# Kernel optimization log

Hardware: AMD Instinct MI355X
Metric: run time of the kernel (lower is better)

## Reference

```python
import jax, jax.numpy as jnp
import numpy as np

N = 100000      # nodes
E = 1600000     # edges (avg degree 16)
D_IN, D_H, D_Z = 128, 64, 32
BN_EPS = 1e-5


def setup_inputs() -> dict:
    key = jax.random.key(0)
    ks = jax.random.split(key, 16)
    lin = lambda k, i, o: jax.random.normal(k, (i, o), jnp.float32) / np.sqrt(i).astype(np.float32)
    return {
        "x": jax.random.normal(ks[0], (N, D_IN), jnp.float32),
        "edge_index": jax.random.randint(ks[1], (2, E), 0, N),
        "edge_attr": jax.random.uniform(ks[2], (E,), jnp.float32),
        "W_in": lin(ks[3], D_IN, D_H), "b_in": jnp.zeros((D_H,), jnp.float32),
        "W1": lin(ks[4], D_H, D_H),   "b1": jnp.zeros((D_H,), jnp.float32),
        "W2": lin(ks[5], D_H, D_H),   "b2": jnp.zeros((D_H,), jnp.float32),
        "Wmu": lin(ks[6], D_H, D_Z),  "bmu": jnp.zeros((D_Z,), jnp.float32),
        "Wlv": lin(ks[7], D_H, D_Z),  "blv": jnp.zeros((D_Z,), jnp.float32),
        "g1": jnp.ones((D_H,), jnp.float32), "be1": jnp.zeros((D_H,), jnp.float32),
        "g2": jnp.ones((D_H,), jnp.float32), "be2": jnp.zeros((D_H,), jnp.float32),
    }


def gcn_conv(h, W, b, src, dst, ew):
    # standard GCNConv: linear transform, then sym-normalized weighted aggregation
    # with self-loops of weight 1.
    h = h @ W + b                                   # [N, F_out]
    deg = jax.ops.segment_sum(ew, dst, num_segments=N) + 1.0   # self-loop -> deg >= 1
    dinv = jax.lax.rsqrt(deg)                       # [N]
    coef = dinv[src] * dinv[dst] * ew               # [E]
    agg = jax.ops.segment_sum(h[src] * coef[:, None], dst, num_segments=N)
    return agg + h * (dinv * dinv)[:, None]         # add self-loop contribution


def batch_norm(h, g, b):
    m = h.mean(axis=0)
    v = h.var(axis=0)
    return g * (h - m) * jax.lax.rsqrt(v + BN_EPS) + b


def reference(x, edge_index, edge_attr, W_in, b_in, W1, b1, W2, b2,
              Wmu, bmu, Wlv, blv, g1, be1, g2, be2):
    src, dst = edge_index[0], edge_index[1]
    h = x @ W_in + b_in
    h = gcn_conv(h, W1, b1, src, dst, edge_attr)
    h = jax.nn.relu(batch_norm(h, g1, be1))         # dropout = identity (eval)
    h = gcn_conv(h, W2, b2, src, dst, edge_attr)
    h = jax.nn.relu(batch_norm(h, g2, be2))
    mu = gcn_conv(h, Wmu, bmu, src, dst, edge_attr)
    logvar = gcn_conv(h, Wlv, blv, src, dst, edge_attr)
    return (mu, logvar)
```

## Files before the change

kernel.cpp:

```cpp
#include <hip/hip_runtime.h>

#define NN 100000
#define NE 1600000

__global__ __launch_bounds__(256) void k_degpack(const int* __restrict__ dst,
    const float* __restrict__ ew, unsigned long long* __restrict__ packed,
    unsigned char* __restrict__ rank) {
  int e = blockIdx.x * 256 + threadIdx.x;
  if (e < NE) {
    int d = dst[e];
    unsigned long long rec = (1ULL << 40) |
        (unsigned long long)__float2uint_rn(ew[e] * 16777216.0f);
    unsigned long long old = atomicAdd(&packed[d], rec);
    rank[e] = (unsigned char)(old >> 40);
  }
}

__global__ __launch_bounds__(256) void k_unpack(const unsigned long long* __restrict__ packed,
    float* __restrict__ dinv, int* __restrict__ cnt) {
  int i = blockIdx.x * 256 + threadIdx.x;
  if (i < NN) {
    unsigned long long v = packed[i];
    cnt[i] = (int)(v >> 40);
    float deg = (float)(v & ((1ULL << 40) - 1)) * (1.0f / 16777216.0f);
    dinv[i] = rsqrtf(deg + 1.0f);
  }
}

__global__ __launch_bounds__(256) void k_scan1(const int* __restrict__ cnt,
    int* __restrict__ indptr, int* __restrict__ bsum) {
  __shared__ int sd[256];
  int t = threadIdx.x, i = blockIdx.x * 256 + t;
  int v = (i < NN) ? cnt[i] : 0;
  sd[t] = v; __syncthreads();
  #pragma unroll
  for (int o = 1; o < 256; o <<= 1) {
    int x = (t >= o) ? sd[t - o] : 0;
    __syncthreads(); sd[t] += x; __syncthreads();
  }
  if (i < NN) indptr[i] = sd[t] - v;
  if (t == 255) bsum[blockIdx.x] = sd[255];
}

__global__ __launch_bounds__(512) void k_scan2(const int* __restrict__ bsum,
    int* __restrict__ boff, int nb) {
  __shared__ int sd[512];
  int t = threadIdx.x;
  int v = (t < nb) ? bsum[t] : 0;
  sd[t] = v; __syncthreads();
  #pragma unroll
  for (int o = 1; o < 512; o <<= 1) {
    int x = (t >= o) ? sd[t - o] : 0;
    __syncthreads(); sd[t] += x; __syncthreads();
  }
  if (t < nb) boff[t] = sd[t] - v;
}

__global__ __launch_bounds__(256) void k_scan3(int* __restrict__ indptr,
    const int* __restrict__ boff) {
  int i = blockIdx.x * 256 + threadIdx.x;
  if (i < NN) {
    indptr[i] = indptr[i] + boff[i >> 8];
  } else if (i == NN) {
    indptr[NN] = NE;
  }
}

__global__ __launch_bounds__(256) void k_fill(const int* __restrict__ src,
    const int* __restrict__ dst, const float* __restrict__ ew,
    const float* __restrict__ dinv, const int* __restrict__ indptr,
    const unsigned char* __restrict__ rank, int2* __restrict__ edges) {
  int e = blockIdx.x * 256 + threadIdx.x;
  if (e < NE) {
    int s = src[e], d = dst[e];
    int p = indptr[d] + (int)rank[e];
    float coef = dinv[s] * dinv[d] * ew[e];
    edges[p] = make_int2(s, __float_as_int(coef));
  }
}

template<int K, int RPT, bool BN>
__global__ __launch_bounds__(256) void k_lin(const float* __restrict__ in,
    const float* __restrict__ W, const float* __restrict__ bias,
    const float* __restrict__ stats, const float* __restrict__ g,
    const float* __restrict__ be, float* __restrict__ out) {
  constexpr int ROWS = 16 * RPT, RS = ROWS + 4;
  __shared__ __align__(16) float Wl[K * 64];
  __shared__ __align__(16) float rlT[K * RS];
  __shared__ __align__(16) float bl[64];
  __shared__ float bnscale[BN ? K : 1], bnshift[BN ? K : 1];
  int t = threadIdx.x;
  int r0 = blockIdx.x * ROWS;
  for (int i = t; i < K * 64; i += 256) Wl[i] = W[i];
  if (t < 64) bl[t] = bias[t];
  if constexpr (BN) {
    if (t < K) {
      const float invn = 1.0f / (float)NN;
      float m = stats[t] * invn;
      float v = stats[64 + t] * invn - m * m;
      float sc = g[t] * rsqrtf(v + 1e-5f);
      bnscale[t] = sc;
      bnshift[t] = be[t] - m * sc;
    }
    __syncthreads();
  }
  for (int i = t; i < ROWS * K; i += 256) {
    int r = i / K, k = i - r * K;
    int row = r0 + r;
    float v = (row < NN) ? in[(size_t)row * K + k] : 0.f;
    if constexpr (BN) {
      v = v * bnscale[k] + bnshift[k];
      v = v > 0.f ? v : 0.f;
    }
    rlT[k * RS + r] = v;
  }
  __syncthreads();
  int tc = t & 15, tr = t >> 4;
  float4 bv = *(const float4*)&bl[tc * 4];
  float acc[RPT][4];
  #pragma unroll
  for (int j = 0; j < RPT; j++) { acc[j][0] = bv.x; acc[j][1] = bv.y; acc[j][2] = bv.z; acc[j][3] = bv.w; }
  for (int k = 0; k < K; k++) {
    float4 wv = *(const float4*)&Wl[k * 64 + tc * 4];
    float rv[RPT];
    if constexpr (RPT == 4) {
      float4 r4 = *(const float4*)&rlT[k * RS + tr * 4];
      rv[0] = r4.x; rv[1] = r4.y; rv[2] = r4.z; rv[3] = r4.w;
    } else {
      float2 r2 = *(const float2*)&rlT[k * RS + tr * 2];
      rv[0] = r2.x; rv[1] = r2.y;
    }
    #pragma unroll
    for (int j = 0; j < RPT; j++) {
      acc[j][0] += rv[j] * wv.x;
      acc[j][1] += rv[j] * wv.y;
      acc[j][2] += rv[j] * wv.z;
      acc[j][3] += rv[j] * wv.w;
    }
  }
  #pragma unroll
  for (int j = 0; j < RPT; j++) {
    int row = r0 + tr * RPT + j;
    if (row < NN) {
      float4 o = make_float4(acc[j][0], acc[j][1], acc[j][2], acc[j][3]);
      *(float4*)&out[(size_t)row * 64 + tc * 4] = o;
    }
  }
}

__global__ __launch_bounds__(256) void k_linz(const float* __restrict__ in,
    const float* __restrict__ Wmu, const float* __restrict__ bmu,
    const float* __restrict__ Wlv, const float* __restrict__ blv,
    const float* __restrict__ stats, const float* __restrict__ g,
    const float* __restrict__ be, float* __restrict__ out) {
  constexpr int K = 64, RPT = 4, ROWS = 64, RS = 68;
  __shared__ __align__(16) float Wl[K * 64];
  __shared__ __align__(16) float rlT[K * RS];
  __shared__ __align__(16) float bl[64];
  __shared__ float bnscale[K], bnshift[K];
  int t = threadIdx.x;
  int r0 = blockIdx.x * ROWS;
  for (int i = t; i < K * 64; i += 256) {
    int k = i >> 6, c = i & 63;
    Wl[i] = (c < 32) ? Wmu[k * 32 + c] : Wlv[k * 32 + c - 32];
  }
  if (t < 64) bl[t] = (t < 32) ? bmu[t] : blv[t - 32];
  if (t < K) {
    const float invn = 1.0f / (float)NN;
    float m = stats[t] * invn;
    float v = stats[64 + t] * invn - m * m;
    float sc = g[t] * rsqrtf(v + 1e-5f);
    bnscale[t] = sc;
    bnshift[t] = be[t] - m * sc;
  }
  __syncthreads();
  for (int i = t; i < ROWS * K; i += 256) {
    int r = i / K, k = i - r * K;
    int row = r0 + r;
    float v = (row < NN) ? in[(size_t)row * K + k] : 0.f;
    v = v * bnscale[k] + bnshift[k];
    rlT[k * RS + r] = v > 0.f ? v : 0.f;
  }
  __syncthreads();
  int tc = t & 15, tr = t >> 4;
  float4 bv = *(const float4*)&bl[tc * 4];
  float acc[RPT][4];
  #pragma unroll
  for (int j = 0; j < RPT; j++) { acc[j][0] = bv.x; acc[j][1] = bv.y; acc[j][2] = bv.z; acc[j][3] = bv.w; }
  for (int k = 0; k < K; k++) {
    float4 wv = *(const float4*)&Wl[k * 64 + tc * 4];
    float4 r4 = *(const float4*)&rlT[k * RS + tr * 4];
    float rv[4] = { r4.x, r4.y, r4.z, r4.w };
    #pragma unroll
    for (int j = 0; j < RPT; j++) {
      acc[j][0] += rv[j] * wv.x;
      acc[j][1] += rv[j] * wv.y;
      acc[j][2] += rv[j] * wv.z;
      acc[j][3] += rv[j] * wv.w;
    }
  }
  #pragma unroll
  for (int j = 0; j < RPT; j++) {
    int row = r0 + tr * RPT + j;
    if (row < NN) {
      float4 o = make_float4(acc[j][0], acc[j][1], acc[j][2], acc[j][3]);
      *(float4*)&out[(size_t)row * 64 + tc * 4] = o;
    }
  }
}

template<bool FINAL>
__global__ __launch_bounds__(256) void k_gather2(const float2* __restrict__ h,
    const float* __restrict__ dinv, const int* __restrict__ indptr,
    const int2* __restrict__ edges, float* __restrict__ out) {
  int wid = (blockIdx.x * 256 + threadIdx.x) >> 6;
  int lane = threadIdx.x & 63;
  int half = lane >> 5, sub = lane & 31;
  int i = wid * 2 + half;
  if (i >= NN) return;
  int e0 = indptr[i], e1 = indptr[i + 1];
  float di = dinv[i];
  float2 hv = h[(size_t)i * 32 + sub];
  float2 acc = make_float2(hv.x * di * di, hv.y * di * di);
  int e = e0;
  for (; e + 8 <= e1; e += 8) {
    int2 r0 = edges[e];
    int2 r1 = edges[e + 1];
    int2 r2 = edges[e + 2];
    int2 r3 = edges[e + 3];
    int2 r4 = edges[e + 4];
    int2 r5 = edges[e + 5];
    int2 r6 = edges[e + 6];
    int2 r7 = edges[e + 7];
    float2 v0 = h[(size_t)r0.x * 32 + sub];
    float2 v1 = h[(size_t)r1.x * 32 + sub];
    float2 v2 = h[(size_t)r2.x * 32 + sub];
    float2 v3 = h[(size_t)r3.x * 32 + sub];
    float2 v4 = h[(size_t)r4.x * 32 + sub];
    float2 v5 = h[(size_t)r5.x * 32 + sub];
    float2 v6 = h[(size_t)r6.x * 32 + sub];
    float2 v7 = h[(size_t)r7.x * 32 + sub];
    float c0 = __int_as_float(r0.y), c1 = __int_as_float(r1.y);
    float c2 = __int_as_float(r2.y), c3 = __int_as_float(r3.y);
    float c4 = __int_as_float(r4.y), c5 = __int_as_float(r5.y);
    float c6 = __int_as_float(r6.y), c7 = __int_as_float(r7.y);
    acc.x += v0.x * c0; acc.y += v0.y * c0;
    acc.x += v1.x * c1; acc.y += v1.y * c1;
    acc.x += v2.x * c2; acc.y += v2.y * c2;
    acc.x += v3.x * c3; acc.y += v3.y * c3;
    acc.x += v4.x * c4; acc.y += v4.y * c4;
    acc.x += v5.x * c5; acc.y += v5.y * c5;
    acc.x += v6.x * c6; acc.y += v6.y * c6;
    acc.x += v7.x * c7; acc.y += v7.y * c7;
  }
  for (; e + 2 <= e1; e += 2) {
    int2 ra = edges[e];
    int2 rb = edges[e + 1];
    float2 va = h[(size_t)ra.x * 32 + sub];
    float2 vb = h[(size_t)rb.x * 32 + sub];
    float ca = __int_as_float(ra.y), cb = __int_as_float(rb.y);
    acc.x += va.x * ca; acc.y += va.y * ca;
    acc.x += vb.x * cb; acc.y += vb.y * cb;
  }
  if (e < e1) {
    int2 r = edges[e];
    float2 v = h[(size_t)r.x * 32 + sub];
    float c = __int_as_float(r.y);
    acc.x += v.x * c; acc.y += v.y * c;
  }
  if (!FINAL) {
    *(float2*)&out[(size_t)i * 64 + sub * 2] = acc;
  } else {
    int c0 = sub * 2;
    if (sub < 16) {
      *(float2*)&out[(size_t)i * 32 + c0] = acc;
    } else {
      *(float2*)&out[(size_t)NN * 32 + (size_t)i * 32 + (c0 - 32)] = acc;
    }
  }
}

__global__ __launch_bounds__(256) void k_bnstats(const float* __restrict__ h,
    float* __restrict__ stats) {
  __shared__ float s1[256], s2[256];
  int t = threadIdx.x, c = t & 63, rg = t >> 6;
  float a1 = 0.f, a2 = 0.f;
  for (int row = blockIdx.x * 4 + rg; row < NN; row += gridDim.x * 4) {
    float v = h[(size_t)row * 64 + c];
    a1 += v; a2 += v * v;
  }
  s1[t] = a1; s2[t] = a2; __syncthreads();
  if (rg == 0) {
    a1 = s1[c] + s1[64 + c] + s1[128 + c] + s1[192 + c];
    a2 = s2[c] + s2[64 + c] + s2[128 + c] + s2[192 + c];
    atomicAdd(&stats[c], a1);
    atomicAdd(&stats[64 + c], a2);
  }
}

extern "C" void kernel_launch(void* const* d_in, const int* in_sizes, int n_in,
                              void* d_out, int out_size, void* d_ws, size_t ws_size,
                              hipStream_t stream) {
  (void)in_sizes; (void)n_in; (void)out_size; (void)ws_size;
  const float* x    = (const float*)d_in[0];
  const int*   ei   = (const int*)d_in[1];
  const float* ew   = (const float*)d_in[2];
  const float* W_in = (const float*)d_in[3];
  const float* b_in = (const float*)d_in[4];
  const float* W1   = (const float*)d_in[5];
  const float* b1   = (const float*)d_in[6];
  const float* W2   = (const float*)d_in[7];
  const float* b2   = (const float*)d_in[8];
  const float* Wmu  = (const float*)d_in[9];
  const float* bmu  = (const float*)d_in[10];
  const float* Wlv  = (const float*)d_in[11];
  const float* blv  = (const float*)d_in[12];
  const float* g1   = (const float*)d_in[13];
  const float* be1  = (const float*)d_in[14];
  const float* g2   = (const float*)d_in[15];
  const float* be2  = (const float*)d_in[16];
  const int* src = ei;
  const int* dst = ei + NE;
  float* out = (float*)d_out;

  char* p = (char*)d_ws;
  auto carve = [&](size_t bytes) { void* r = (void*)p; p += (bytes + 255) & ~(size_t)255; return r; };
  float* A      = (float*)carve((size_t)NN * 64 * 4);
  float* B      = (float*)carve((size_t)NN * 64 * 4);
  unsigned long long* packed = (unsigned long long*)carve((size_t)NN * 8);
  float* dinv   = (float*)carve((size_t)NN * 4);
  int*   cnt    = (int*)carve((size_t)NN * 4);
  int*   indptr = (int*)carve((size_t)(NN + 1) * 4);
  unsigned char* rank = (unsigned char*)carve((size_t)NE);
  int2*  edges  = (int2*)carve((size_t)NE * 8);
  int*   bsum   = (int*)carve(512 * 4);
  int*   boff   = (int*)carve(512 * 4);
  float* stats1 = (float*)carve(128 * 4);
  float* stats2 = (float*)carve(128 * 4);

  const int nbE = (NE + 255) / 256;
  const int nbN = (NN + 255) / 256;
  const int gLin128 = (NN + 31) / 32;
  const int gLin64  = (NN + 63) / 64;
  const int gWave2  = ((NN + 1) / 2 * 64 + 255) / 256;

  hipMemsetAsync(packed, 0, (size_t)NN * 8, stream);
  k_degpack<<<nbE, 256, 0, stream>>>(dst, ew, packed, rank);
  k_unpack<<<nbN, 256, 0, stream>>>(packed, dinv, cnt);
  k_scan1<<<nbN, 256, 0, stream>>>(cnt, indptr, bsum);
  k_scan2<<<1, 512, 0, stream>>>(bsum, boff, nbN);
  k_scan3<<<nbN, 256, 0, stream>>>(indptr, boff);
  k_fill<<<nbE, 256, 0, stream>>>(src, dst, ew, dinv, indptr, rank, edges);

  k_lin<128, 2, false><<<gLin128, 256, 0, stream>>>(x, W_in, b_in, nullptr, nullptr, nullptr, A);
  k_lin<64, 4, false><<<gLin64, 256, 0, stream>>>(A, W1, b1, nullptr, nullptr, nullptr, B);
  k_gather2<false><<<gWave2, 256, 0, stream>>>((const float2*)B, dinv, indptr, edges, A);
  hipMemsetAsync(stats1, 0, 128 * 4, stream);
  k_bnstats<<<256, 256, 0, stream>>>(A, stats1);
  k_lin<64, 4, true><<<gLin64, 256, 0, stream>>>(A, W2, b2, stats1, g1, be1, B);
  k_gather2<false><<<gWave2, 256, 0, stream>>>((const float2*)B, dinv, indptr, edges, A);
  hipMemsetAsync(stats2, 0, 128 * 4, stream);
  k_bnstats<<<256, 256, 0, stream>>>(A, stats2);
  k_linz<<<gLin64, 256, 0, stream>>>(A, Wmu, bmu, Wlv, blv, stats2, g2, be2, B);
  k_gather2<true><<<gWave2, 256, 0, stream>>>((const float2*)B, dinv, indptr, edges, out);
}
```

Baseline: 612.5 us.

## Store intermediate node features as bf16 and gather four nodes per wave

Intermediate feature buffers A/B move from fp32 to bf16, halving the bytes moved by the linear, stats and gather kernels. The gather kernel is reworked so each wave handles four nodes, with 16 lanes each reading ushort4 (64 channels), and bnstats is vectorized over ushort4. This targets the memory-bound random gathers over 1.6M edges. It adds bf16 rounding error to the hidden activations and outputs.

```diff
diff --git a/kernel.cpp b/kernel.cpp
--- a/kernel.cpp
+++ b/kernel.cpp
@@ -2,6 +2,15 @@
 
 #define NN 100000
 #define NE 1600000
+
+__device__ __forceinline__ float b2f(unsigned short u) {
+  return __uint_as_float(((unsigned)u) << 16);
+}
+__device__ __forceinline__ unsigned short f2bf(float f) {
+  unsigned u = __float_as_uint(f);
+  u += 0x7fffu + ((u >> 16) & 1u);
+  return (unsigned short)(u >> 16);
+}
 
 __global__ __launch_bounds__(256) void k_degpack(const int* __restrict__ dst,
     const float* __restrict__ ew, unsigned long long* __restrict__ packed,
@@ -79,22 +88,22 @@
   }
 }
 
-template<int K, int RPT, bool BN>
-__global__ __launch_bounds__(256) void k_lin(const float* __restrict__ in,
+template<int K, int RPT, bool BN, bool BFIN>
+__global__ __launch_bounds__(256) void k_lin(const void* __restrict__ inv,
     const float* __restrict__ W, const float* __restrict__ bias,
     const float* __restrict__ stats, const float* __restrict__ g,
-    const float* __restrict__ be, float* __restrict__ out) {
+    const float* __restrict__ be, unsigned short* __restrict__ out) {
   constexpr int ROWS = 16 * RPT, RS = ROWS + 4;
   __shared__ __align__(16) float Wl[K * 64];
   __shared__ __align__(16) float rlT[K * RS];
   __shared__ __align__(16) float bl[64];
-  __shared__ float bnscale[BN ? K : 1], bnshift[BN ? K : 1];
+  __shared__ float bnscale[BN ? 64 : 1], bnshift[BN ? 64 : 1];
   int t = threadIdx.x;
   int r0 = blockIdx.x * ROWS;
   for (int i = t; i < K * 64; i += 256) Wl[i] = W[i];
   if (t < 64) bl[t] = bias[t];
   if constexpr (BN) {
-    if (t < K) {
+    if (t < 64) {
       const float invn = 1.0f / (float)NN;
       float m = stats[t] * invn;
       float v = stats[64 + t] * invn - m * m;
@@ -104,15 +113,32 @@
     }
     __syncthreads();
   }
-  for (int i = t; i < ROWS * K; i += 256) {
-    int r = i / K, k = i - r * K;
-    int row = r0 + r;
-    float v = (row < NN) ? in[(size_t)row * K + k] : 0.f;
-    if constexpr (BN) {
-      v = v * bnscale[k] + bnshift[k];
-      v = v > 0.f ? v : 0.f;
-    }
-    rlT[k * RS + r] = v;
+  if constexpr (BFIN) {
+    const unsigned short* in = (const unsigned short*)inv;
+    for (int i = t; i < ROWS * (K / 4); i += 256) {
+      int r = i / (K / 4), k0 = (i % (K / 4)) * 4;
+      int row = r0 + r;
+      ushort4 u = (row < NN) ? *(const ushort4*)&in[(size_t)row * K + k0]
+                             : make_ushort4(0, 0, 0, 0);
+      float v0 = b2f(u.x), v1 = b2f(u.y), v2 = b2f(u.z), v3 = b2f(u.w);
+      if constexpr (BN) {
+        v0 = v0 * bnscale[k0] + bnshift[k0];         v0 = v0 > 0.f ? v0 : 0.f;
+        v1 = v1 * bnscale[k0 + 1] + bnshift[k0 + 1]; v1 = v1 > 0.f ? v1 : 0.f;
+        v2 = v2 * bnscale[k0 + 2] + bnshift[k0 + 2]; v2 = v2 > 0.f ? v2 : 0.f;
+        v3 = v3 * bnscale[k0 + 3] + bnshift[k0 + 3]; v3 = v3 > 0.f ? v3 : 0.f;
+      }
+      rlT[(k0 + 0) * RS + r] = v0;
+      rlT[(k0 + 1) * RS + r] = v1;
+      rlT[(k0 + 2) * RS + r] = v2;
+      rlT[(k0 + 3) * RS + r] = v3;
+    }
+  } else {
+    const float* in = (const float*)inv;
+    for (int i = t; i < ROWS * K; i += 256) {
+      int r = i / K, k = i - r * K;
+      int row = r0 + r;
+      rlT[k * RS + r] = (row < NN) ? in[(size_t)row * K + k] : 0.f;
+    }
   }
   __syncthreads();
   int tc = t & 15, tr = t >> 4;
@@ -142,22 +168,23 @@
   for (int j = 0; j < RPT; j++) {
     int row = r0 + tr * RPT + j;
     if (row < NN) {
-      float4 o = make_float4(acc[j][0], acc[j][1], acc[j][2], acc[j][3]);
-      *(float4*)&out[(size_t)row * 64 + tc * 4] = o;
-    }
-  }
-}
-
-__global__ __launch_bounds__(256) void k_linz(const float* __restrict__ in,
+      ushort4 o = make_ushort4(f2bf(acc[j][0]), f2bf(acc[j][1]),
+                               f2bf(acc[j][2]), f2bf(acc[j][3]));
+      *(ushort4*)&out[(size_t)row * 64 + tc * 4] = o;
+    }
+  }
+}
+
+__global__ __launch_bounds__(256) void k_linz(const unsigned short* __restrict__ in,
     const float* __restrict__ Wmu, const float* __restrict__ bmu,
     const float* __restrict__ Wlv, const float* __restrict__ blv,
     const float* __restrict__ stats, const float* __restrict__ g,
-    const float* __restrict__ be, float* __restrict__ out) {
+    const float* __restrict__ be, unsigned short* __restrict__ out) {
   constexpr int K = 64, RPT = 4, ROWS = 64, RS = 68;
   __shared__ __align__(16) float Wl[K * 64];
   __shared__ __align__(16) float rlT[K * RS];
   __shared__ __align__(16) float bl[64];
-  __shared__ float bnscale[K], bnshift[K];
+  __shared__ float bnscale[64], bnshift[64];
   int t = threadIdx.x;
   int r0 = blockIdx.x * ROWS;
   for (int i = t; i < K * 64; i += 256) {
@@ -165,7 +192,7 @@
     Wl[i] = (c < 32) ? Wmu[k * 32 + c] : Wlv[k * 32 + c - 32];
   }
   if (t < 64) bl[t] = (t < 32) ? bmu[t] : blv[t - 32];
-  if (t < K) {
+  if (t < 64) {
     const float invn = 1.0f / (float)NN;
     float m = stats[t] * invn;
     float v = stats[64 + t] * invn - m * m;
@@ -174,12 +201,19 @@
     bnshift[t] = be[t] - m * sc;
   }
   __syncthreads();
-  for (int i = t; i < ROWS * K; i += 256) {
-    int r = i / K, k = i - r * K;
+  for (int i = t; i < ROWS * 16; i += 256) {
+    int r = i / 16, k0 = (i & 15) * 4;
     int row = r0 + r;
-    float v = (row < NN) ? in[(size_t)row * K + k] : 0.f;
-    v = v * bnscale[k] + bnshift[k];
-    rlT[k * RS + r] = v > 0.f ? v : 0.f;
+    ushort4 u = (row < NN) ? *(const ushort4*)&in[(size_t)row * 64 + k0]
+                           : make_ushort4(0, 0, 0, 0);
+    float v0 = b2f(u.x) * bnscale[k0] + bnshift[k0];
+    float v1 = b2f(u.y) * bnscale[k0 + 1] + bnshift[k0 + 1];
+    float v2 = b2f(u.z) * bnscale[k0 + 2] + bnshift[k0 + 2];
+    float v3 = b2f(u.w) * bnscale[k0 + 3] + bnshift[k0 + 3];
+    rlT[(k0 + 0) * RS + r] = v0 > 0.f ? v0 : 0.f;
+    rlT[(k0 + 1) * RS + r] = v1 > 0.f ? v1 : 0.f;
+    rlT[(k0 + 2) * RS + r] = v2 > 0.f ? v2 : 0.f;
+    rlT[(k0 + 3) * RS + r] = v3 > 0.f ? v3 : 0.f;
   }
   __syncthreads();
   int tc = t & 15, tr = t >> 4;
@@ -203,98 +237,97 @@
   for (int j = 0; j < RPT; j++) {
     int row = r0 + tr * RPT + j;
     if (row < NN) {
-      float4 o = make_float4(acc[j][0], acc[j][1], acc[j][2], acc[j][3]);
-      *(float4*)&out[(size_t)row * 64 + tc * 4] = o;
+      ushort4 o = make_ushort4(f2bf(acc[j][0]), f2bf(acc[j][1]),
+                               f2bf(acc[j][2]), f2bf(acc[j][3]));
+      *(ushort4*)&out[(size_t)row * 64 + tc * 4] = o;
     }
   }
 }
 
 template<bool FINAL>
-__global__ __launch_bounds__(256) void k_gather2(const float2* __restrict__ h,
+__global__ __launch_bounds__(256) void k_gather4(const unsigned short* __restrict__ h,
     const float* __restrict__ dinv, const int* __restrict__ indptr,
-    const int2* __restrict__ edges, float* __restrict__ out) {
+    const int2* __restrict__ edges, void* __restrict__ outp) {
   int wid = (blockIdx.x * 256 + threadIdx.x) >> 6;
   int lane = threadIdx.x & 63;
-  int half = lane >> 5, sub = lane & 31;
-  int i = wid * 2 + half;
+  int q = lane >> 4, sub = lane & 15;
+  int i = wid * 4 + q;
   if (i >= NN) return;
   int e0 = indptr[i], e1 = indptr[i + 1];
-  float di = dinv[i];
-  float2 hv = h[(size_t)i * 32 + sub];
-  float2 acc = make_float2(hv.x * di * di, hv.y * di * di);
+  float di = dinv[i], di2 = di * di;
+  ushort4 hv = *(const ushort4*)&h[(size_t)i * 64 + sub * 4];
+  float a0 = b2f(hv.x) * di2, a1 = b2f(hv.y) * di2;
+  float a2 = b2f(hv.z) * di2, a3 = b2f(hv.w) * di2;
   int e = e0;
   for (; e + 8 <= e1; e += 8) {
-    int2 r0 = edges[e];
-    int2 r1 = edges[e + 1];
-    int2 r2 = edges[e + 2];
-    int2 r3 = edges[e + 3];
-    int2 r4 = edges[e + 4];
-    int2 r5 = edges[e + 5];
-    int2 r6 = edges[e + 6];
-    int2 r7 = edges[e + 7];
-    float2 v0 = h[(size_t)r0.x * 32 + sub];
-    float2 v1 = h[(size_t)r1.x * 32 + sub];
-    float2 v2 = h[(size_t)r2.x * 32 + sub];
-    float2 v3 = h[(size_t)r3.x * 32 + sub];
-    float2 v4 = h[(size_t)r4.x * 32 + sub];
-    float2 v5 = h[(size_t)r5.x * 32 + sub];
-    float2 v6 = h[(size_t)r6.x * 32 + sub];
-    float2 v7 = h[(size_t)r7.x * 32 + sub];
+    int2 r0 = edges[e],     r1 = edges[e + 1], r2 = edges[e + 2], r3 = edges[e + 3];
+    int2 r4 = edges[e + 4], r5 = edges[e + 5], r6 = edges[e + 6], r7 = edges[e + 7];
+    ushort4 v0 = *(const ushort4*)&h[(size_t)r0.x * 64 + sub * 4];
+    ushort4 v1 = *(const ushort4*)&h[(size_t)r1.x * 64 + sub * 4];
+    ushort4 v2 = *(const ushort4*)&h[(size_t)r2.x * 64 + sub * 4];
+    ushort4 v3 = *(const ushort4*)&h[(size_t)r3.x * 64 + sub * 4];
+    ushort4 v4 = *(const ushort4*)&h[(size_t)r4.x * 64 + sub * 4];
+    ushort4 v5 = *(const ushort4*)&h[(size_t)r5.x * 64 + sub * 4];
+    ushort4 v6 = *(const ushort4*)&h[(size_t)r6.x * 64 + sub * 4];
+    ushort4 v7 = *(const ushort4*)&h[(size_t)r7.x * 64 + sub * 4];
     float c0 = __int_as_float(r0.y), c1 = __int_as_float(r1.y);
     float c2 = __int_as_float(r2.y), c3 = __int_as_float(r3.y);
     float c4 = __int_as_float(r4.y), c5 = __int_as_float(r5.y);
     float c6 = __int_as_float(r6.y), c7 = __int_as_float(r7.y);
-    acc.x += v0.x * c0; acc.y += v0.y * c0;
-    acc.x += v1.x * c1; acc.y += v1.y * c1;
-    acc.x += v2.x * c2; acc.y += v2.y * c2;
-    acc.x += v3.x * c3; acc.y += v3.y * c3;
-    acc.x += v4.x * c4; acc.y += v4.y * c4;
-    acc.x += v5.x * c5; acc.y += v5.y * c5;
-    acc.x += v6.x * c6; acc.y += v6.y * c6;
-    acc.x += v7.x * c7; acc.y += v7.y * c7;
-  }
-  for (; e + 2 <= e1; e += 2) {
-    int2 ra = edges[e];
-    int2 rb = edges[e + 1];
-    float2 va = h[(size_t)ra.x * 32 + sub];
-    float2 vb = h[(size_t)rb.x * 32 + sub];
-    float ca = __int_as_float(ra.y), cb = __int_as_float(rb.y);
-    acc.x += va.x * ca; acc.y += va.y * ca;
-    acc.x += vb.x * cb; acc.y += vb.y * cb;
-  }
-  if (e < e1) {
+    a0 += b2f(v0.x) * c0; a1 += b2f(v0.y) * c0; a2 += b2f(v0.z) * c0; a3 += b2f(v0.w) * c0;
+    a0 += b2f(v1.x) * c1; a1 += b2f(v1.y) * c1; a2 += b2f(v1.z) * c1; a3 += b2f(v1.w) * c1;
+    a0 += b2f(v2.x) * c2; a1 += b2f(v2.y) * c2; a2 += b2f(v2.z) * c2; a3 += b2f(v2.w) * c2;
+    a0 += b2f(v3.x) * c3; a1 += b2f(v3.y) * c3; a2 += b2f(v3.z) * c3; a3 += b2f(v3.w) * c3;
+    a0 += b2f(v4.x) * c4; a1 += b2f(v4.y) * c4; a2 += b2f(v4.z) * c4; a3 += b2f(v4.w) * c4;
+    a0 += b2f(v5.x) * c5; a1 += b2f(v5.y) * c5; a2 += b2f(v5.z) * c5; a3 += b2f(v5.w) * c5;
+    a0 += b2f(v6.x) * c6; a1 += b2f(v6.y) * c6; a2 += b2f(v6.z) * c6; a3 += b2f(v6.w) * c6;
+    a0 += b2f(v7.x) * c7; a1 += b2f(v7.y) * c7; a2 += b2f(v7.z) * c7; a3 += b2f(v7.w) * c7;
+  }
+  for (; e < e1; e++) {
     int2 r = edges[e];
-    float2 v = h[(size_t)r.x * 32 + sub];
+    ushort4 v = *(const ushort4*)&h[(size_t)r.x * 64 + sub * 4];
     float c = __int_as_float(r.y);
-    acc.x += v.x * c; acc.y += v.y * c;
+    a0 += b2f(v.x) * c; a1 += b2f(v.y) * c; a2 += b2f(v.z) * c; a3 += b2f(v.w) * c;
   }
   if (!FINAL) {
-    *(float2*)&out[(size_t)i * 64 + sub * 2] = acc;
+    unsigned short* out = (unsigned short*)outp;
+    ushort4 o = make_ushort4(f2bf(a0), f2bf(a1), f2bf(a2), f2bf(a3));
+    *(ushort4*)&out[(size_t)i * 64 + sub * 4] = o;
   } else {
-    int c0 = sub * 2;
-    if (sub < 16) {
-      *(float2*)&out[(size_t)i * 32 + c0] = acc;
+    float* out = (float*)outp;
+    float4 o = make_float4(a0, a1, a2, a3);
+    if (sub < 8) {
+      *(float4*)&out[(size_t)i * 32 + sub * 4] = o;
     } else {
-      *(float2*)&out[(size_t)NN * 32 + (size_t)i * 32 + (c0 - 32)] = acc;
-    }
-  }
-}
-
-__global__ __launch_bounds__(256) void k_bnstats(const float* __restrict__ h,
+      *(float4*)&out[(size_t)NN * 32 + (size_t)i * 32 + (sub * 4 - 32)] = o;
+    }
+  }
+}
+
+__global__ __launch_bounds__(256) void k_bnstats(const unsigned short* __restrict__ h,
     float* __restrict__ stats) {
-  __shared__ float s1[256], s2[256];
-  int t = threadIdx.x, c = t & 63, rg = t >> 6;
-  float a1 = 0.f, a2 = 0.f;
-  for (int row = blockIdx.x * 4 + rg; row < NN; row += gridDim.x * 4) {
-    float v = h[(size_t)row * 64 + c];
-    a1 += v; a2 += v * v;
-  }
-  s1[t] = a1; s2[t] = a2; __syncthreads();
-  if (rg == 0) {
-    a1 = s1[c] + s1[64 + c] + s1[128 + c] + s1[192 + c];
-    a2 = s2[c] + s2[64 + c] + s2[128 + c] + s2[192 + c];
-    atomicAdd(&stats[c], a1);
-    atomicAdd(&stats[64 + c], a2);
+  __shared__ float sh1[16][68], sh2[16][68];
+  int t = threadIdx.x;
+  int cg = (t & 15) * 4, rg = t >> 4;
+  float s10 = 0.f, s11 = 0.f, s12 = 0.f, s13 = 0.f;
+  float s20 = 0.f, s21 = 0.f, s22 = 0.f, s23 = 0.f;
+  for (int row = blockIdx.x * 16 + rg; row < NN; row += gridDim.x * 16) {
+    ushort4 u = *(const ushort4*)&h[(size_t)row * 64 + cg];
+    float v0 = b2f(u.x), v1 = b2f(u.y), v2 = b2f(u.z), v3 = b2f(u.w);
+    s10 += v0; s20 += v0 * v0;
+    s11 += v1; s21 += v1 * v1;
+    s12 += v2; s22 += v2 * v2;
+    s13 += v3; s23 += v3 * v3;
+  }
+  sh1[rg][cg] = s10; sh1[rg][cg + 1] = s11; sh1[rg][cg + 2] = s12; sh1[rg][cg + 3] = s13;
+  sh2[rg][cg] = s20; sh2[rg][cg + 1] = s21; sh2[rg][cg + 2] = s22; sh2[rg][cg + 3] = s23;
+  __syncthreads();
+  if (t < 64) {
+    float a1 = 0.f, a2 = 0.f;
+    #pragma unroll
+    for (int r = 0; r < 16; r++) { a1 += sh1[r][t]; a2 += sh2[r][t]; }
+    atomicAdd(&stats[t], a1);
+    atomicAdd(&stats[64 + t], a2);
   }
 }
 
@@ -325,8 +358,8 @@
 
   char* p = (char*)d_ws;
   auto carve = [&](size_t bytes) { void* r = (void*)p; p += (bytes + 255) & ~(size_t)255; return r; };
-  float* A      = (float*)carve((size_t)NN * 64 * 4);
-  float* B      = (float*)carve((size_t)NN * 64 * 4);
+  unsigned short* A = (unsigned short*)carve((size_t)NN * 64 * 2);
+  unsigned short* B = (unsigned short*)carve((size_t)NN * 64 * 2);
   unsigned long long* packed = (unsigned long long*)carve((size_t)NN * 8);
   float* dinv   = (float*)carve((size_t)NN * 4);
   int*   cnt    = (int*)carve((size_t)NN * 4);
@@ -342,7 +375,7 @@
   const int nbN = (NN + 255) / 256;
   const int gLin128 = (NN + 31) / 32;
   const int gLin64  = (NN + 63) / 64;
-  const int gWave2  = ((NN + 1) / 2 * 64 + 255) / 256;
+  const int gWave4  = (NN + 15) / 16;
 
   hipMemsetAsync(packed, 0, (size_t)NN * 8, stream);
   k_degpack<<<nbE, 256, 0, stream>>>(dst, ew, packed, rank);
@@ -352,15 +385,15 @@
   k_scan3<<<nbN, 256, 0, stream>>>(indptr, boff);
   k_fill<<<nbE, 256, 0, stream>>>(src, dst, ew, dinv, indptr, rank, edges);
 
-  k_lin<128, 2, false><<<gLin128, 256, 0, stream>>>(x, W_in, b_in, nullptr, nullptr, nullptr, A);
-  k_lin<64, 4, false><<<gLin64, 256, 0, stream>>>(A, W1, b1, nullptr, nullptr, nullptr, B);
-  k_gather2<false><<<gWave2, 256, 0, stream>>>((const float2*)B, dinv, indptr, edges, A);
+  k_lin<128, 2, false, false><<<gLin128, 256, 0, stream>>>(x, W_in, b_in, nullptr, nullptr, nullptr, A);
+  k_lin<64, 4, false, true><<<gLin64, 256, 0, stream>>>(A, W1, b1, nullptr, nullptr, nullptr, B);
+  k_gather4<false><<<gWave4, 256, 0, stream>>>(B, dinv, indptr, edges, A);
   hipMemsetAsync(stats1, 0, 128 * 4, stream);
   k_bnstats<<<256, 256, 0, stream>>>(A, stats1);
-  k_lin<64, 4, true><<<gLin64, 256, 0, stream>>>(A, W2, b2, stats1, g1, be1, B);
-  k_gather2<false><<<gWave2, 256, 0, stream>>>((const float2*)B, dinv, indptr, edges, A);
+  k_lin<64, 4, true, true><<<gLin64, 256, 0, stream>>>(A, W2, b2, stats1, g1, be1, B);
+  k_gather4<false><<<gWave4, 256, 0, stream>>>(B, dinv, indptr, edges, A);
   hipMemsetAsync(stats2, 0, 128 * 4, stream);
   k_bnstats<<<256, 256, 0, stream>>>(A, stats2);
   k_linz<<<gLin64, 256, 0, stream>>>(A, Wmu, bmu, Wlv, blv, stats2, g2, be2, B);
-  k_gather2<true><<<gWave2, 256, 0, stream>>>((const float2*)B, dinv, indptr, edges, out);
-}
+  k_gather4<true><<<gWave4, 256, 0, stream>>>(B, dinv, indptr, edges, out);
+}
```

After: 497.4 us. 18.8% less time.
